# Optimization experiments

Hardware: AMD Instinct MI355X
Metric: run time of the kernel (lower is better)

## Reference

```python
import jax, jax.numpy as jnp
import numpy as np
import math

B, S, D = 2, 2048, 1024
HQ, HKV = 16, 4
HD = D // HQ          # 64
N_REP = HQ // HKV     # 4
WINDOW = 256
ROPE_BASE = 10000.0


def _rope(x):
    # x: [b, s, h, hd]; interleaved-pair rotary (torchtune style)
    s, hd = x.shape[1], x.shape[-1]
    inv_freq = 1.0 / (ROPE_BASE ** (jnp.arange(0, hd, 2, dtype=jnp.float32) / hd))
    ang = jnp.arange(s, dtype=jnp.float32)[:, None] * inv_freq          # [s, hd/2]
    cos = jnp.cos(ang)[None, :, None, :].astype(x.dtype)
    sin = jnp.sin(ang)[None, :, None, :].astype(x.dtype)
    x1, x2 = x[..., ::2], x[..., 1::2]
    out = jnp.stack([x1 * cos - x2 * sin, x1 * sin + x2 * cos], axis=-1)
    return out.reshape(x.shape)


def setup_inputs() -> dict:
    key = jax.random.key(0)
    ks = jax.random.split(key, 5)
    sc = 0.02
    return {
        "x": jax.random.normal(ks[0], (B, S, D), dtype=jnp.float32),
        "Wq": jax.random.normal(ks[1], (D, HQ * HD), dtype=jnp.float32) * sc,
        "Wk": jax.random.normal(ks[2], (D, HKV * HD), dtype=jnp.float32) * sc,
        "Wv": jax.random.normal(ks[3], (D, HKV * HD), dtype=jnp.float32) * sc,
        "Wo": jax.random.normal(ks[4], (HQ * HD, D), dtype=jnp.float32) * sc,
    }


def reference(x, Wq, Wk, Wv, Wo):
    b, s, _ = x.shape
    xq = (x @ Wq).reshape(b, s, HQ, HD)
    xk = (x @ Wk).reshape(b, s, HKV, HD)
    xv = (x @ Wv).reshape(b, s, HKV, HD)

    xq = _rope(xq)
    xk = _rope(xk)

    # GQA: repeat kv heads to match query heads
    keys = jnp.repeat(xk, N_REP, axis=2)    # [b, s, HQ, HD]
    values = jnp.repeat(xv, N_REP, axis=2)

    scores = jnp.einsum("bqhd,bkhd->bhqk", xq, keys) / math.sqrt(HD)

    # symmetric sliding window: keep |i - j| <= WINDOW // 2
    idx = jnp.arange(s)
    mask = jnp.abs(idx[:, None] - idx[None, :]) <= (WINDOW // 2)  # [s, s]
    scores = jnp.where(mask[None, None], scores, -jnp.inf)

    attn = jax.nn.softmax(scores.astype(jnp.float32), axis=-1).astype(xq.dtype)
    ctx = jnp.einsum("bhqk,bkhd->bqhd", attn, values).reshape(b, s, HQ * HD)
    return ctx @ Wo
```

## Files before the change

### kernel.cpp

```cpp
#include <hip/hip_runtime.h>

typedef unsigned short u16;
typedef unsigned int u32;
typedef __attribute__((ext_vector_type(8))) short bfrag;
typedef __attribute__((ext_vector_type(4))) float f32x4;

#define S_LEN 2048
#define DMODEL 1024
#define NHQ 16
#define NHKV 4
#define HD 64
#define HALFW 128
#define ROWS 4096
#define QSCALE 0.1803368801111244f

__device__ __forceinline__ u16 f2b(float f) {
  u32 x = __float_as_uint(f);
  return (u16)((x + 0x7fffu + ((x >> 16) & 1u)) >> 16);
}

__device__ __forceinline__ u32 cvtpk(float lo, float hi) {
  u32 r;
  asm("v_cvt_pk_bf16_f32 %0, %1, %2" : "=v"(r) : "v"(lo), "v"(hi));
  return r;
}

__device__ __forceinline__ float fexp(float x) {
  float r;
  asm("v_exp_f32 %0, %1" : "=v"(r) : "v"(x));
  return r;
}

__global__ void prep_k(const float* __restrict__ x, const float* __restrict__ Wq,
                       const float* __restrict__ Wk, const float* __restrict__ Wv,
                       const float* __restrict__ Wo, u16* __restrict__ xb,
                       u16* __restrict__ Wcat_t, u16* __restrict__ Wo_t,
                       float2* __restrict__ csT) {
  __shared__ float tile[32][33];
  int y = blockIdx.y;
  int tid = threadIdx.y * 32 + threadIdx.x;
  if (y >= 88) {
    int i = (((y - 88) * 32 + blockIdx.x) * 256 + tid) * 4;
    float4 v = *reinterpret_cast<const float4*>(x + i);
    uint2 p;
    p.x = (u32)f2b(v.x) | ((u32)f2b(v.y) << 16);
    p.y = (u32)f2b(v.z) | ((u32)f2b(v.w) << 16);
    *reinterpret_cast<uint2*>(xb + i) = p;
    return;
  }
  if (y >= 80) {
    int idx = ((y - 80) * 32 + blockIdx.x) * 256 + tid;
    int s = idx >> 5, i = idx & 31;
    double inv = pow(10000.0, -(double)(2 * i) / 64.0);
    double ang = (double)s * inv;
    csT[idx] = make_float2((float)cos(ang), (float)sin(ang));
    return;
  }
  int k0 = blockIdx.x * 32;
  const float* src; u16* dst; int ncols, n0;
  if (y < 32)      { src = Wq; dst = Wcat_t;                       ncols = 1024; n0 = y * 32; }
  else if (y < 40) { src = Wk; dst = Wcat_t + (size_t)1024 * 1024; ncols = 256;  n0 = (y - 32) * 32; }
  else if (y < 48) { src = Wv; dst = Wcat_t + (size_t)1280 * 1024; ncols = 256;  n0 = (y - 40) * 32; }
  else             { src = Wo; dst = Wo_t;                         ncols = 1024; n0 = (y - 48) * 32; }
  int tx = threadIdx.x, ty = threadIdx.y;
#pragma unroll
  for (int j = 0; j < 4; ++j)
    tile[ty + 8 * j][tx] = src[(size_t)(k0 + ty + 8 * j) * ncols + n0 + tx];
  __syncthreads();
#pragma unroll
  for (int j = 0; j < 4; ++j)
    dst[(size_t)(n0 + ty + 8 * j) * 1024 + k0 + tx] = f2b(tile[tx][ty + 8 * j]);
}

__device__ __forceinline__ void gemm_core(const u16* __restrict__ A, const u16* __restrict__ Bt,
                                          int m0, int n0, int wave, int lane,
                                          f32x4 acc[4][2]) {
  __shared__ u16 lds_a[2 * 128 * 64];
  __shared__ u16 lds_b[2 * 64 * 64];
  int t = wave * 64 + lane;
  int g = lane >> 4, col = lane & 15;
  int wm = wave >> 1, wn = wave & 1;
  int r8 = t >> 3, slot = (t & 7) ^ (r8 & 7);
  const u16* Ab = A + (size_t)(m0 + r8) * 1024 + slot * 8;
  const u16* Bb = Bt + (size_t)(n0 + r8) * 1024 + slot * 8;
  int c7 = col & 7;
  int aoff0 = (wm * 64 + col) * 64;
  int boff0 = (wn * 32 + col) * 64;
#pragma unroll
  for (int j = 0; j < 4; ++j)
    __builtin_amdgcn_global_load_lds(
        (const __attribute__((address_space(1))) u32*)(Ab + (size_t)j * 32768),
        (__attribute__((address_space(3))) u32*)(lds_a + j * 2048 + wave * 512), 16, 0, 0);
#pragma unroll
  for (int j = 0; j < 2; ++j)
    __builtin_amdgcn_global_load_lds(
        (const __attribute__((address_space(1))) u32*)(Bb + (size_t)j * 32768),
        (__attribute__((address_space(3))) u32*)(lds_b + j * 2048 + wave * 512), 16, 0, 0);
  __syncthreads();
  for (int kt = 0; kt < 16; ++kt) {
    int cur = kt & 1;
    if (kt < 15) {
      int ko = (kt + 1) * 64;
      u16* la = lds_a + (cur ^ 1) * 8192;
      u16* lb = lds_b + (cur ^ 1) * 4096;
#pragma unroll
      for (int j = 0; j < 4; ++j)
        __builtin_amdgcn_global_load_lds(
            (const __attribute__((address_space(1))) u32*)(Ab + (size_t)j * 32768 + ko),
            (__attribute__((address_space(3))) u32*)(la + j * 2048 + wave * 512), 16, 0, 0);
#pragma unroll
      for (int j = 0; j < 2; ++j)
        __builtin_amdgcn_global_load_lds(
            (const __attribute__((address_space(1))) u32*)(Bb + (size_t)j * 32768 + ko),
            (__attribute__((address_space(3))) u32*)(lb + j * 2048 + wave * 512), 16, 0, 0);
    }
    const u16* la = lds_a + cur * 8192;
    const u16* lb = lds_b + cur * 4096;
#pragma unroll
    for (int sub = 0; sub < 2; ++sub) {
      int sa = ((sub * 4 + g) ^ c7) * 8;
      bfrag af[4], bf[2];
#pragma unroll
      for (int mi = 0; mi < 4; ++mi)
        af[mi] = *reinterpret_cast<const bfrag*>(&la[aoff0 + mi * 1024 + sa]);
#pragma unroll
      for (int ni = 0; ni < 2; ++ni)
        bf[ni] = *reinterpret_cast<const bfrag*>(&lb[boff0 + ni * 1024 + sa]);
#pragma unroll
      for (int mi = 0; mi < 4; ++mi)
#pragma unroll
        for (int ni = 0; ni < 2; ++ni)
          acc[mi][ni] = __builtin_amdgcn_mfma_f32_16x16x32_bf16(af[mi], bf[ni], acc[mi][ni], 0, 0, 0);
    }
    if (kt < 15) __syncthreads();
  }
}

__global__ __launch_bounds__(256) void gemm_qkv_k(const u16* __restrict__ A, const u16* __restrict__ Bt,
                                                  const float2* __restrict__ csT,
                                                  u16* __restrict__ Qr, u16* __restrict__ Kr,
                                                  u16* __restrict__ Vt) {
  int t = threadIdx.x;
  int wave = t >> 6, lane = t & 63;
  int g = lane >> 4, col = lane & 15;
  int m0 = blockIdx.y * 128, n0 = blockIdx.x * 64;
  int wm = wave >> 1, wn = wave & 1;
  f32x4 acc[4][2] = {};
  gemm_core(A, Bt, m0, n0, wave, lane, acc);
  bool odd = (col & 1) != 0;
#pragma unroll
  for (int mi = 0; mi < 4; ++mi)
#pragma unroll
    for (int ni = 0; ni < 2; ++ni) {
      int cg = n0 + wn * 32 + ni * 16 + col;
      int rowbase = m0 + wm * 64 + mi * 16 + g * 4;
      if (cg < 1024) {
        int hq = cg >> 6, d = cg & 63, i = d >> 1;
        u16* dst = Qr + ((size_t)((rowbase >> 11) * NHQ + hq) * S_LEN + (rowbase & 2047)) * HD + d;
#pragma unroll
        for (int r = 0; r < 4; ++r) {
          int s = (rowbase + r) & 2047;
          float v = acc[mi][ni][r];
          float pv = __shfl_xor(v, 1);
          float2 cs = csT[s * 32 + i];
          float o = odd ? (pv * cs.y + v * cs.x) : (v * cs.x - pv * cs.y);
          dst[(size_t)r * HD] = f2b(o * QSCALE);
        }
      } else if (cg < 1280) {
        int j = cg - 1024;
        int kh = j >> 6, d = j & 63, i = d >> 1;
        u16* dst = Kr + ((size_t)((rowbase >> 11) * NHKV + kh) * S_LEN + (rowbase & 2047)) * HD + d;
#pragma unroll
        for (int r = 0; r < 4; ++r) {
          int s = (rowbase + r) & 2047;
          float v = acc[mi][ni][r];
          float pv = __shfl_xor(v, 1);
          float2 cs = csT[s * 32 + i];
          float o = odd ? (pv * cs.y + v * cs.x) : (v * cs.x - pv * cs.y);
          dst[(size_t)r * HD] = f2b(o);
        }
      } else {
        int j = cg - 1280;
        int kh = j >> 6, d = j & 63;
        int b = rowbase >> 11, s0 = rowbase & 2047;
        uint2 o;
        o.x = (u32)f2b(acc[mi][ni][0]) | ((u32)f2b(acc[mi][ni][1]) << 16);
        o.y = (u32)f2b(acc[mi][ni][2]) | ((u32)f2b(acc[mi][ni][3]) << 16);
        *reinterpret_cast<uint2*>(Vt + ((size_t)(b * NHKV + kh) * HD + d) * S_LEN + s0) = o;
      }
    }
}

__global__ __launch_bounds__(256) void gemm_bt_k(const u16* __restrict__ A, const u16* __restrict__ Bt,
                                                 float* __restrict__ C, int N) {
  int t = threadIdx.x;
  int wave = t >> 6, lane = t & 63;
  int g = lane >> 4, col = lane & 15;
  int m0 = blockIdx.y * 128, n0 = blockIdx.x * 64;
  int wm = wave >> 1, wn = wave & 1;
  f32x4 acc[4][2] = {};
  gemm_core(A, Bt, m0, n0, wave, lane, acc);
#pragma unroll
  for (int mi = 0; mi < 4; ++mi)
#pragma unroll
    for (int ni = 0; ni < 2; ++ni) {
      int row = m0 + wm * 64 + mi * 16 + g * 4;
      int cc = n0 + wn * 32 + ni * 16 + col;
#pragma unroll
      for (int r = 0; r < 4; ++r)
        C[(size_t)(row + r) * N + cc] = acc[mi][ni][r];
    }
}

__global__ __launch_bounds__(256) void attn_k(const u16* __restrict__ Qr, const u16* __restrict__ Kr,
                                              const u16* __restrict__ Vt, u16* __restrict__ ctx) {
  int bid = blockIdx.x;
  int qblk = bid & 15, h = (bid >> 4) & 15, b = bid >> 8;
  int wave = threadIdx.x >> 6, lane = threadIdx.x & 63;
  int g = lane >> 4, col = lane & 15;
  int kv = h >> 2;
  int q0 = qblk * 128 + wave * 32;
  const u16* Qb = Qr + (size_t)(b * NHQ + h) * S_LEN * HD;
  const u16* Kb = Kr + (size_t)(b * NHKV + kv) * S_LEN * HD;
  const u16* Vb = Vt + (size_t)(b * NHKV + kv) * HD * S_LEN;
  bfrag qf[2][2];
#pragma unroll
  for (int qg = 0; qg < 2; ++qg) {
    qf[qg][0] = *reinterpret_cast<const bfrag*>(&Qb[(size_t)(q0 + qg * 16 + col) * HD + 8 * g]);
    qf[qg][1] = *reinterpret_cast<const bfrag*>(&Qb[(size_t)(q0 + qg * 16 + col) * HD + 32 + 8 * g]);
  }
  f32x4 octx[2][4] = {};
  float lacc[2] = {0.f, 0.f};
  int qi[2] = {q0 + col, q0 + 16 + col};
  bool hi5 = (threadIdx.x & 32) != 0;
  int l0b = (col + ((lane >> 4) & 1) * 32) << 2;
  int l1b = l0b + 64;
  int lo = q0 - HALFW; if (lo < 0) lo = 0; lo &= ~31;
  int hi = q0 + 32 + HALFW; if (hi > S_LEN) hi = S_LEN;
  for (int c0 = lo; c0 < hi; c0 += 32) {
    f32x4 s[2][2] = {};
    __builtin_amdgcn_s_setprio(1);
#pragma unroll
    for (int kt = 0; kt < 2; ++kt)
#pragma unroll
      for (int dh = 0; dh < 2; ++dh) {
        bfrag kf = *reinterpret_cast<const bfrag*>(&Kb[(size_t)(c0 + kt * 16 + col) * HD + 32 * dh + 8 * g]);
        s[0][kt] = __builtin_amdgcn_mfma_f32_16x16x32_bf16(kf, qf[0][dh], s[0][kt], 0, 0, 0);
        s[1][kt] = __builtin_amdgcn_mfma_f32_16x16x32_bf16(kf, qf[1][dh], s[1][kt], 0, 0, 0);
      }
    __builtin_amdgcn_s_setprio(0);
    bool full = (c0 >= q0 + 31 - HALFW) && (c0 + 31 <= q0 + HALFW);
    union { bfrag f; u32 w[4]; } pb[2];
#pragma unroll
    for (int qg = 0; qg < 2; ++qg) {
      float p0[4], p1[4];
      if (full) {
#pragma unroll
        for (int r = 0; r < 4; ++r) { p0[r] = fexp(s[qg][0][r]); p1[r] = fexp(s[qg][1][r]); }
      } else {
        int d0 = c0 + 4 * g - qi[qg] + HALFW;
#pragma unroll
        for (int r = 0; r < 4; ++r) {
          p0[r] = ((u32)(d0 + r) <= 2u * HALFW) ? fexp(s[qg][0][r]) : 0.f;
          p1[r] = ((u32)(d0 + 16 + r) <= 2u * HALFW) ? fexp(s[qg][1][r]) : 0.f;
        }
      }
      lacc[qg] += ((p0[0] + p0[1]) + (p0[2] + p0[3])) + ((p1[0] + p1[1]) + (p1[2] + p1[3]));
      u32 pk0 = cvtpk(p0[0], p0[1]), pk1 = cvtpk(p0[2], p0[3]);
      u32 pk2 = cvtpk(p1[0], p1[1]), pk3 = cvtpk(p1[2], p1[3]);
      u32 a0 = (u32)__builtin_amdgcn_ds_bpermute(l0b, (int)pk0);
      u32 b0 = (u32)__builtin_amdgcn_ds_bpermute(l0b, (int)pk2);
      u32 a1 = (u32)__builtin_amdgcn_ds_bpermute(l0b, (int)pk1);
      u32 b1 = (u32)__builtin_amdgcn_ds_bpermute(l0b, (int)pk3);
      u32 a2 = (u32)__builtin_amdgcn_ds_bpermute(l1b, (int)pk0);
      u32 b2 = (u32)__builtin_amdgcn_ds_bpermute(l1b, (int)pk2);
      u32 a3 = (u32)__builtin_amdgcn_ds_bpermute(l1b, (int)pk1);
      u32 b3 = (u32)__builtin_amdgcn_ds_bpermute(l1b, (int)pk3);
      pb[qg].w[0] = hi5 ? b0 : a0;
      pb[qg].w[1] = hi5 ? b1 : a1;
      pb[qg].w[2] = hi5 ? b2 : a2;
      pb[qg].w[3] = hi5 ? b3 : a3;
    }
    __builtin_amdgcn_s_setprio(1);
#pragma unroll
    for (int n = 0; n < 4; ++n) {
      bfrag vf = *reinterpret_cast<const bfrag*>(&Vb[(size_t)(n * 16 + col) * S_LEN + c0 + 8 * g]);
      octx[0][n] = __builtin_amdgcn_mfma_f32_16x16x32_bf16(vf, pb[0].f, octx[0][n], 0, 0, 0);
      octx[1][n] = __builtin_amdgcn_mfma_f32_16x16x32_bf16(vf, pb[1].f, octx[1][n], 0, 0, 0);
    }
    __builtin_amdgcn_s_setprio(0);
  }
#pragma unroll
  for (int qg = 0; qg < 2; ++qg) {
    float l = lacc[qg] + __shfl_xor(lacc[qg], 16);
    l += __shfl_xor(l, 32);
    float linv = __builtin_amdgcn_rcpf(l);
    u16* cb = ctx + (size_t)b * S_LEN * DMODEL + (size_t)(q0 + qg * 16 + col) * DMODEL + h * HD;
#pragma unroll
    for (int n = 0; n < 4; ++n) {
      uint2 o;
      o.x = cvtpk(octx[qg][n][0] * linv, octx[qg][n][1] * linv);
      o.y = cvtpk(octx[qg][n][2] * linv, octx[qg][n][3] * linv);
      *reinterpret_cast<uint2*>(cb + n * 16 + 4 * g) = o;
    }
  }
}

extern "C" void kernel_launch(void* const* d_in, const int* in_sizes, int n_in,
                              void* d_out, int out_size, void* d_ws, size_t ws_size,
                              hipStream_t stream) {
  (void)in_sizes; (void)n_in; (void)out_size; (void)ws_size;
  const float* x  = (const float*)d_in[0];
  const float* Wq = (const float*)d_in[1];
  const float* Wk = (const float*)d_in[2];
  const float* Wv = (const float*)d_in[3];
  const float* Wo = (const float*)d_in[4];
  char* ws = (char*)d_ws;
  u16*    xb     = (u16*)(ws + 0);
  u16*    Wcat_t = (u16*)(ws + 8388608);
  u16*    Wo_t   = (u16*)(ws + 11534336);
  u16*    Qr     = (u16*)(ws + 13631488);
  u16*    Kr     = (u16*)(ws + 22020096);
  u16*    Vt     = (u16*)(ws + 24117248);
  u16*    ctxb   = (u16*)(ws + 26214400);
  float2* csT    = (float2*)(ws + 34603008);

  prep_k<<<dim3(32, 216), dim3(32, 8), 0, stream>>>(x, Wq, Wk, Wv, Wo, xb, Wcat_t, Wo_t, csT);
  gemm_qkv_k<<<dim3(24, 32), 256, 0, stream>>>(xb, Wcat_t, csT, Qr, Kr, Vt);
  attn_k<<<512, 256, 0, stream>>>(Qr, Kr, Vt, ctxb);
  gemm_bt_k<<<dim3(16, 32), 256, 0, stream>>>(ctxb, Wo_t, (float*)d_out, 1024);
}
```

Before: 75.70 us.

## Share K/V tiles across GQA heads via double-buffered async LDS staging

Each attention block now maps its four waves to the four query heads that share one KV head over the same 32 query rows. Previously each wave covered a different query range of a single head. K and V chunks are loaded once per block straight into LDS with global_load_lds, using an XOR swizzle against bank conflicts. The LDS is double-buffered so the next chunk loads while the current one is computed. This cuts redundant global/L2 reads of K/V by the GQA factor, but adds a block-wide barrier per chunk and depends on the barrier waiting for the async LDS loads.

```diff
diff --git a/kernel.cpp b/kernel.cpp
--- a/kernel.cpp
+++ b/kernel.cpp
@@ -214,12 +214,15 @@
 
 __global__ __launch_bounds__(256) void attn_k(const u16* __restrict__ Qr, const u16* __restrict__ Kr,
                                               const u16* __restrict__ Vt, u16* __restrict__ ctx) {
+  __shared__ u16 lds_k[2][32 * 64];
+  __shared__ u16 lds_v[2][64 * 32];
   int bid = blockIdx.x;
-  int qblk = bid & 15, h = (bid >> 4) & 15, b = bid >> 8;
-  int wave = threadIdx.x >> 6, lane = threadIdx.x & 63;
+  int qblk = bid & 63, kv = (bid >> 6) & 3, b = bid >> 8;
+  int tid = threadIdx.x;
+  int wave = tid >> 6, lane = tid & 63;
   int g = lane >> 4, col = lane & 15;
-  int kv = h >> 2;
-  int q0 = qblk * 128 + wave * 32;
+  int h = kv * 4 + wave;
+  int q0 = qblk * 32;
   const u16* Qb = Qr + (size_t)(b * NHQ + h) * S_LEN * HD;
   const u16* Kb = Kr + (size_t)(b * NHKV + kv) * S_LEN * HD;
   const u16* Vb = Vt + (size_t)(b * NHKV + kv) * HD * S_LEN;
@@ -232,19 +235,37 @@
   f32x4 octx[2][4] = {};
   float lacc[2] = {0.f, 0.f};
   int qi[2] = {q0 + col, q0 + 16 + col};
-  bool hi5 = (threadIdx.x & 32) != 0;
+  bool hi5 = (tid & 32) != 0;
   int l0b = (col + ((lane >> 4) & 1) * 32) << 2;
   int l1b = l0b + 64;
   int lo = q0 - HALFW; if (lo < 0) lo = 0; lo &= ~31;
   int hi = q0 + 32 + HALFW; if (hi > S_LEN) hi = S_LEN;
-  for (int c0 = lo; c0 < hi; c0 += 32) {
+  int nt = (hi - lo) >> 5;
+  int kr = tid >> 3, ks = (tid & 7) ^ (kr & 7);
+  int vr = tid >> 2, vs = (tid & 3) ^ (vr & 3);
+  const u16* Ksrc = Kb + (size_t)kr * HD + ks * 8;
+  const u16* Vsrc = Vb + (size_t)vr * S_LEN + vs * 8;
+  int c7 = col & 7, c3 = col & 3;
+
+  auto STAGE = [&](int buf, int c0) {
+    __builtin_amdgcn_global_load_lds(
+        (const __attribute__((address_space(1))) u32*)(Ksrc + (size_t)c0 * HD),
+        (__attribute__((address_space(3))) u32*)(&lds_k[buf][wave * 512]), 16, 0, 0);
+    __builtin_amdgcn_global_load_lds(
+        (const __attribute__((address_space(1))) u32*)(Vsrc + c0),
+        (__attribute__((address_space(3))) u32*)(&lds_v[buf][wave * 512]), 16, 0, 0);
+  };
+  auto COMPUTE = [&](int buf, int c0) {
+    const u16* lk = lds_k[buf];
+    const u16* lv = lds_v[buf];
     f32x4 s[2][2] = {};
     __builtin_amdgcn_s_setprio(1);
 #pragma unroll
     for (int kt = 0; kt < 2; ++kt)
 #pragma unroll
       for (int dh = 0; dh < 2; ++dh) {
-        bfrag kf = *reinterpret_cast<const bfrag*>(&Kb[(size_t)(c0 + kt * 16 + col) * HD + 32 * dh + 8 * g]);
+        bfrag kf = *reinterpret_cast<const bfrag*>(
+            &lk[(kt * 16 + col) * 64 + (((dh << 2) | g) ^ c7) * 8]);
         s[0][kt] = __builtin_amdgcn_mfma_f32_16x16x32_bf16(kf, qf[0][dh], s[0][kt], 0, 0, 0);
         s[1][kt] = __builtin_amdgcn_mfma_f32_16x16x32_bf16(kf, qf[1][dh], s[1][kt], 0, 0, 0);
       }
@@ -284,11 +305,21 @@
     __builtin_amdgcn_s_setprio(1);
 #pragma unroll
     for (int n = 0; n < 4; ++n) {
-      bfrag vf = *reinterpret_cast<const bfrag*>(&Vb[(size_t)(n * 16 + col) * S_LEN + c0 + 8 * g]);
+      bfrag vf = *reinterpret_cast<const bfrag*>(
+          &lv[(n * 16 + col) * 32 + (g ^ c3) * 8]);
       octx[0][n] = __builtin_amdgcn_mfma_f32_16x16x32_bf16(vf, pb[0].f, octx[0][n], 0, 0, 0);
       octx[1][n] = __builtin_amdgcn_mfma_f32_16x16x32_bf16(vf, pb[1].f, octx[1][n], 0, 0, 0);
     }
     __builtin_amdgcn_s_setprio(0);
+  };
+
+  STAGE(0, lo);
+  __syncthreads();
+  for (int i = 0; i < nt; ++i) {
+    int cur = i & 1;
+    if (i + 1 < nt) STAGE(cur ^ 1, lo + (i + 1) * 32);
+    COMPUTE(cur, lo + i * 32);
+    if (i + 1 < nt) __syncthreads();
   }
 #pragma unroll
   for (int qg = 0; qg < 2; ++qg) {
```

New measurement: 69.70 us. -7.9%, faster.
